# Kernel tuning notes

Measured on AMD Instinct MI355X. Metric: run time of the kernel, lower is better.

The kernel has to match this reference:

```python
import jax, jax.numpy as jnp
import numpy as np

Y_DIM = 100  # number of speakers (one-hot dim)


def _conv1d(x, w, b, stride=2, pad=1):
    # x: [B, Cin, L], w: [Cout, Cin, K] (torch Conv1d layout)
    out = jax.lax.conv_general_dilated(x, w, (stride,), [(pad, pad)],
                                       dimension_numbers=('NCH', 'OIH', 'NCH'))
    return out + b[None, :, None]


def _deconv1d(x, w, b, stride=2, pad=1):
    # w: [Cin, Cout, K] (torch ConvTranspose1d layout)
    k = w.shape[-1]
    wt = jnp.flip(w, -1).transpose(1, 0, 2)  # -> [Cout, Cin, K]
    out = jax.lax.conv_general_dilated(x, wt, (1,), [(k - 1 - pad, k - 1 - pad)],
                                       lhs_dilation=(stride,),
                                       dimension_numbers=('NCH', 'OIH', 'NCH'))
    return out + b[None, :, None]


def _forward(x, enc, codebook, emb_w, emb_b, dec, mu_w, mu_b, spk_idx):
    h = x[:, None, :]                         # [B, 1, 512]
    for w, b in enc:
        h = jax.nn.relu(_conv1d(h, w, b))
    z = h[:, 0, :]                            # [B, 64]
    # 0.5 * ||z - c||^2 for all codes, via expansion (fused cdist)
    d = 0.5 * (jnp.sum(z * z, 1, keepdims=True)
               - 2.0 * z @ codebook.T
               + jnp.sum(codebook * codebook, 1)[None, :])  # [B, K]
    idx = jnp.argmin(d, axis=1)               # first-min tie-break matches strict '<' loop
    code = codebook[idx]                      # [B, 64]
    y = jax.nn.one_hot(spk_idx, Y_DIM, dtype=x.dtype)
    dec_in = jnp.concatenate([code, y], 1) @ emb_w.T + emb_b  # [B, 64]
    h = dec_in[:, None, :]
    for w, b in dec:
        h = jax.nn.relu(_deconv1d(h, w, b))
    out = (h @ mu_w.T + mu_b)[:, 0, :]        # [B, 512]
    return z, code, out


def setup_inputs() -> dict:
    key = jax.random.key(0)
    ks = jax.random.split(key, 20)
    B, L, D, K, Y = 8192, 512, 64, 512, 100
    s = 0.1
    return {
        'x': jax.random.normal(ks[0], (B, L), jnp.float32),
        'enc_w0': jax.random.normal(ks[1], (32, 1, 4), jnp.float32) * s,
        'enc_b0': jnp.zeros((32,), jnp.float32),
        'enc_w1': jax.random.normal(ks[2], (32, 32, 4), jnp.float32) * s,
        'enc_b1': jnp.zeros((32,), jnp.float32),
        'enc_w2': jax.random.normal(ks[3], (1, 32, 4), jnp.float32) * s,
        'enc_b2': jnp.zeros((1,), jnp.float32),
        'codebook': jax.random.normal(ks[4], (K, D), jnp.float32) * s,
        'emb_w': jax.random.normal(ks[5], (D, Y + D), jnp.float32) * s,
        'emb_b': jnp.zeros((D,), jnp.float32),
        'dec_w0': jax.random.normal(ks[6], (1, 32, 4), jnp.float32) * s,
        'dec_b0': jnp.zeros((32,), jnp.float32),
        'dec_w1': jax.random.normal(ks[7], (32, 32, 4), jnp.float32) * s,
        'dec_b1': jnp.zeros((32,), jnp.float32),
        'dec_w2': jax.random.normal(ks[8], (32, 1, 4), jnp.float32) * s,
        'dec_b2': jnp.zeros((1,), jnp.float32),
        'mu_w': jax.random.normal(ks[9], (L, L), jnp.float32) * s,
        'mu_b': jnp.zeros((L,), jnp.float32),
        'spk_idx': jax.random.randint(ks[10], (B,), 0, Y, jnp.int32),
    }


def reference(x, enc_w0, enc_b0, enc_w1, enc_b1, enc_w2, enc_b2, codebook,
              emb_w, emb_b, dec_w0, dec_b0, dec_w1, dec_b1, dec_w2, dec_b2,
              mu_w, mu_b, spk_idx):
    enc = [(enc_w0, enc_b0), (enc_w1, enc_b1), (enc_w2, enc_b2)]
    dec = [(dec_w0, dec_b0), (dec_w1, dec_b1), (dec_w2, dec_b2)]
    return _forward(x, enc, codebook, emb_w, emb_b, dec, mu_w, mu_b, spk_idx)
```

## Files before the change

kernel.cpp:

```cpp
#include <hip/hip_runtime.h>
#include <hip/hip_bf16.h>

__device__ __forceinline__ float bits2f(unsigned int b) {
    union { unsigned int u; float f; } v; v.u = b; return v.f;
}
__device__ __forceinline__ unsigned short f2bf_bits(float f) {
    union { float f; unsigned int u; } v; v.f = f;
    return (unsigned short)((v.u + 0x7fffu + ((v.u >> 16) & 1u)) >> 16);
}
__device__ __forceinline__ unsigned short f2h_bits(_Float16 h) {
    union { _Float16 f; unsigned short u; } v; v.f = h; return v.u;
}

typedef __attribute__((ext_vector_type(8))) short short8;
typedef __attribute__((ext_vector_type(4))) float f32x4;
typedef _Float16 f16x8 __attribute__((ext_vector_type(8)));

#define AS1 __attribute__((address_space(1)))
#define AS3 __attribute__((address_space(3)))

__device__ __align__(16) unsigned short g_muwb[512 * 512];
__device__ __align__(16) unsigned short g_dec1B[4096];
__device__ __align__(16) unsigned short g_dec2B[5120];
__device__ __align__(16) unsigned short g_encBh[4096];
__device__ __align__(16) unsigned short g_encBl[4096];
__device__ float g_cc[512];
__device__ __align__(16) float g_cbT[64 * 512];
__device__ __align__(16) float g_embwT[164 * 64];

__global__ __launch_bounds__(256)
void k_prep(const float* __restrict__ muw, const float* __restrict__ dw1,
            const float* __restrict__ dw2, const float* __restrict__ ew1,
            const float* __restrict__ cb, const float* __restrict__ embw)
{
    int idx = blockIdx.x * 256 + threadIdx.x;
    if (idx < 262144) { g_muwb[idx] = f2bf_bits(muw[idx]); return; }
    int e = idx - 262144;
    if (e < 4096) {
        const int jsel[4] = {1, 3, 2, 0};
        int pt = e >> 10, o = (e >> 5) & 31, i = e & 31;
        g_dec1B[e] = f2bf_bits(dw1[i * 128 + o * 4 + jsel[pt]]);
        return;
    }
    int f = e - 4096;
    if (f < 5120) {
        int j = f / 320, k = f - j * 320;
        int lam = k >> 5, i = k & 31, q = j >> 1;
        float v = 0.f;
        if ((j & 1) == 0) {
            if (lam == q + 1) v = dw2[4 * i + 1];
            else if (lam == q) v = dw2[4 * i + 3];
        } else {
            if (lam == q + 1) v = dw2[4 * i + 2];
            else if (lam == q + 2) v = dw2[4 * i + 0];
        }
        g_dec2B[f] = f2bf_bits(v);
        return;
    }
    int g = f - 5120;
    if (g < 4096) {
        int j = g >> 10, o = (g >> 5) & 31, i = g & 31;
        float w = ew1[o * 128 + i * 4 + j];
        _Float16 wh = (_Float16)w;
        _Float16 wl = (_Float16)((w - (float)wh) * 2048.0f);
        g_encBh[g] = f2h_bits(wh);
        g_encBl[g] = f2h_bits(wl);
        return;
    }
    int h = g - 4096;
    if (h < 512) {
        const float4* cp = (const float4*)(cb + (size_t)h * 64);
        float cc2 = 0.f;
        #pragma unroll
        for (int q = 0; q < 16; ++q) {
            float4 u = cp[q];
            cc2 += u.x * u.x + u.y * u.y + u.z * u.z + u.w * u.w;
        }
        g_cc[h] = cc2;
        return;
    }
    int m = h - 512;
    if (m < 32768) {
        int d = m >> 9, c = m & 511;
        g_cbT[m] = cb[(size_t)c * 64 + d];
        return;
    }
    int n2 = m - 32768;
    if (n2 < 10496) {
        int k = n2 >> 6, j = n2 & 63;
        g_embwT[n2] = embw[(size_t)j * 164 + k];
    }
}

__global__ __launch_bounds__(256, 2)
void k_encoder(const float* __restrict__ x,
               const float* __restrict__ ew0, const float* __restrict__ eb0,
               const float* __restrict__ eb1,
               const float* __restrict__ ew2, const float* __restrict__ eb2,
               float* __restrict__ z_out)
{
    const int tid  = threadIdx.x;
    const int lane = tid & 63;
    const int w    = tid >> 6;
    const int rloc = w >> 1;
    const int wh   = w & 1;
    const int row  = blockIdx.x * 2 + rloc;

    __shared__ __align__(16) float POOL[2 * 4688];
    float* ws = POOL + rloc * 4688;
    float* xs = ws;
    float* h2 = ws + 520;

    const int r = lane & 15, kc = lane >> 4;
    const float biaN0 = eb1[r], biaN1 = eb1[16 + r];

    const float* xrow = x + (size_t)row * 512;
    #pragma unroll
    for (int q = 0; q < 4; ++q) {
        const int ch = wh * 4 + q;
        xs[3 + lane + 64 * ch] = xrow[lane + 64 * ch];
    }
    if (wh == 0) {
        if (lane < 3) xs[lane] = 0.f;
        h2[(lane >> 1) * 130 + 2 + (lane & 1)] = 0.f;
    } else {
        if (lane < 3) xs[515 + lane] = 0.f;
        if (lane < 2) { int gi = 64 + lane; h2[(gi >> 1) * 130 + 2 + (gi & 1)] = 0.f; }
    }

    f16x8 Bh[2][4], Bl[2][4];
    #pragma unroll
    for (int nt = 0; nt < 2; ++nt)
        #pragma unroll
        for (int j = 0; j < 4; ++j) {
            const int off = (j * 32 + nt * 16 + r) * 32 + kc * 8;
            Bh[nt][j] = *(const f16x8*)(g_encBh + off);
            Bl[nt][j] = *(const f16x8*)(g_encBl + off);
        }
    float4 Wv[8]; float b0v[8];
    #pragma unroll
    for (int i = 0; i < 8; ++i) {
        Wv[i]  = *(const float4*)(ew0 + (kc * 8 + i) * 4);
        b0v[i] = eb0[kc * 8 + i];
    }
    __syncthreads();

    #pragma unroll 2
    for (int mi = 0; mi < 4; ++mi) {
        const int m = 4 * wh + mi;
        const int t2 = m * 16 + r;
        float xw[10];
        {
            const float* xwin = xs + 4 * t2;
            #pragma unroll
            for (int q = 0; q < 10; ++q) xw[q] = xwin[q];
        }
        f16x8 ah0, ah1, ah2, ah3, al0, al1, al2, al3;
        #pragma unroll
        for (int i = 0; i < 8; ++i) {
            const float4 W = Wv[i];
            const float b0 = b0v[i];
            float v0 = fmaxf(b0 + xw[0] * W.x + xw[1] * W.y + xw[2] * W.z + xw[3] * W.w, 0.f);
            float v1 = fmaxf(b0 + xw[2] * W.x + xw[3] * W.y + xw[4] * W.z + xw[5] * W.w, 0.f);
            float v2 = fmaxf(b0 + xw[4] * W.x + xw[5] * W.y + xw[6] * W.z + xw[7] * W.w, 0.f);
            float v3 = fmaxf(b0 + xw[6] * W.x + xw[7] * W.y + xw[8] * W.z + xw[9] * W.w, 0.f);
            _Float16 hh0 = (_Float16)v0, hh1 = (_Float16)v1;
            _Float16 hh2 = (_Float16)v2, hh3 = (_Float16)v3;
            _Float16 ll0 = (_Float16)((v0 - (float)hh0) * 2048.0f);
            _Float16 ll1 = (_Float16)((v1 - (float)hh1) * 2048.0f);
            _Float16 ll2 = (_Float16)((v2 - (float)hh2) * 2048.0f);
            _Float16 ll3 = (_Float16)((v3 - (float)hh3) * 2048.0f);
            ah0[i] = hh0; al0[i] = ll0;
            ah1[i] = hh1; al1[i] = ll1;
            ah2[i] = hh2; al2[i] = ll2;
            ah3[i] = hh3; al3[i] = ll3;
        }
        {
            const f16x8 Z8 = {(_Float16)0.f, (_Float16)0.f, (_Float16)0.f, (_Float16)0.f,
                              (_Float16)0.f, (_Float16)0.f, (_Float16)0.f, (_Float16)0.f};
            if (t2 == 0)   { ah0 = Z8; al0 = Z8; }
            if (t2 == 127) { ah3 = Z8; al3 = Z8; }
        }
        const int t0 = m * 16;
        #pragma unroll
        for (int nt = 0; nt < 2; ++nt) {
            f32x4 ahh = (f32x4){0.f, 0.f, 0.f, 0.f};
            f32x4 am  = (f32x4){0.f, 0.f, 0.f, 0.f};
            f32x4 all_= (f32x4){0.f, 0.f, 0.f, 0.f};
            ahh = __builtin_amdgcn_mfma_f32_16x16x32_f16(ah0, Bh[nt][0], ahh, 0, 0, 0);
            am  = __builtin_amdgcn_mfma_f32_16x16x32_f16(ah0, Bl[nt][0], am,  0, 0, 0);
            am  = __builtin_amdgcn_mfma_f32_16x16x32_f16(al0, Bh[nt][0], am,  0, 0, 0);
            all_= __builtin_amdgcn_mfma_f32_16x16x32_f16(al0, Bl[nt][0], all_,0, 0, 0);
            ahh = __builtin_amdgcn_mfma_f32_16x16x32_f16(ah1, Bh[nt][1], ahh, 0, 0, 0);
            am  = __builtin_amdgcn_mfma_f32_16x16x32_f16(ah1, Bl[nt][1], am,  0, 0, 0);
            am  = __builtin_amdgcn_mfma_f32_16x16x32_f16(al1, Bh[nt][1], am,  0, 0, 0);
            all_= __builtin_amdgcn_mfma_f32_16x16x32_f16(al1, Bl[nt][1], all_,0, 0, 0);
            ahh = __builtin_amdgcn_mfma_f32_16x16x32_f16(ah2, Bh[nt][2], ahh, 0, 0, 0);
            am  = __builtin_amdgcn_mfma_f32_16x16x32_f16(ah2, Bl[nt][2], am,  0, 0, 0);
            am  = __builtin_amdgcn_mfma_f32_16x16x32_f16(al2, Bh[nt][2], am,  0, 0, 0);
            all_= __builtin_amdgcn_mfma_f32_16x16x32_f16(al2, Bl[nt][2], all_,0, 0, 0);
            ahh = __builtin_amdgcn_mfma_f32_16x16x32_f16(ah3, Bh[nt][3], ahh, 0, 0, 0);
            am  = __builtin_amdgcn_mfma_f32_16x16x32_f16(ah3, Bl[nt][3], am,  0, 0, 0);
            am  = __builtin_amdgcn_mfma_f32_16x16x32_f16(al3, Bh[nt][3], am,  0, 0, 0);
            all_= __builtin_amdgcn_mfma_f32_16x16x32_f16(al3, Bl[nt][3], all_,0, 0, 0);
            const float bia = nt ? biaN1 : biaN0;
            float* orow = h2 + (nt * 16 + r) * 130 + 4 + t0 + kc * 4;
            #pragma unroll
            for (int e = 0; e < 4; ++e)
                orow[e] = fmaxf(ahh[e] + 4.8828125e-4f * am[e]
                                + 2.384185791015625e-07f * all_[e] + bia, 0.f);
        }
    }
    __syncthreads();

    if (wh == 0) {
        const int t = lane;
        float pg[4];
        #pragma unroll
        for (int gg = 0; gg < 4; ++gg) {
            float p = 0.f;
            #pragma unroll
            for (int ii = 0; ii < 8; ++ii) {
                const int i = gg * 8 + ii;
                const float4 W = *(const float4*)(ew2 + i * 4);
                const float* hr = h2 + i * 130 + 4;
                p += hr[2 * t - 1] * W.x + hr[2 * t] * W.y
                   + hr[2 * t + 1] * W.z + hr[2 * t + 2] * W.w;
            }
            pg[gg] = p;
        }
        float zv = fmaxf(pg[0] + pg[1] + pg[2] + pg[3] + eb2[0], 0.f);
        z_out[(size_t)row * 64 + t] = zv;
    }
}

__global__ __launch_bounds__(256)
void k_enc_tail(const float* __restrict__ z_in, const float* __restrict__ cb,
                const float* __restrict__ embb,
                const int* __restrict__ spk,
                float* __restrict__ code_out, float* __restrict__ din_g)
{
    const int blk  = blockIdx.x;
    const int tid  = threadIdx.x;
    const int lane = tid & 63;
    const int wv   = tid >> 6;

    __shared__ __align__(16) float zs[8][64];
    __shared__ __align__(16) float csf[8][64];
    __shared__ float zzv[8];
    __shared__ float redv[4][8];
    __shared__ int   redi[4][8];
    __shared__ int   sidxs[8];

    const int jq = tid & 63;
    const int rq = tid >> 6;

    #pragma unroll
    for (int ch = 0; ch < 2; ++ch) {
        const int rr = rq + ch * 4;
        zs[rr][jq] = z_in[((size_t)blk * 8 + rr) * 64 + jq];
    }
    __syncthreads();

    if (tid < 8) {
        float4 zr[16];
        #pragma unroll
        for (int q = 0; q < 16; ++q) zr[q] = *(const float4*)(&zs[tid][4 * q]);
        float u[32];
        #pragma unroll
        for (int q = 0; q < 8; ++q) {
            u[4 * q + 0] = __fadd_rn(__fmul_rn(zr[q].x, zr[q].x), __fmul_rn(zr[q + 8].x, zr[q + 8].x));
            u[4 * q + 1] = __fadd_rn(__fmul_rn(zr[q].y, zr[q].y), __fmul_rn(zr[q + 8].y, zr[q + 8].y));
            u[4 * q + 2] = __fadd_rn(__fmul_rn(zr[q].z, zr[q].z), __fmul_rn(zr[q + 8].z, zr[q + 8].z));
            u[4 * q + 3] = __fadd_rn(__fmul_rn(zr[q].w, zr[q].w), __fmul_rn(zr[q + 8].w, zr[q + 8].w));
        }
        #pragma unroll
        for (int off = 16; off; off >>= 1)
            #pragma unroll
            for (int i = 0; i < off; ++i) u[i] = __fadd_rn(u[i], u[i + off]);
        zzv[tid] = u[0];
    }

    float acc[8][2];
    #pragma unroll
    for (int r2 = 0; r2 < 8; ++r2) { acc[r2][0] = 0.f; acc[r2][1] = 0.f; }

    #pragma unroll 4
    for (int dq = 0; dq < 16; ++dq) {
        float4 zv[8];
        #pragma unroll
        for (int r2 = 0; r2 < 8; ++r2) zv[r2] = *(const float4*)(&zs[r2][4 * dq]);
        #pragma unroll
        for (int dd = 0; dd < 4; ++dd) {
            const int d = 4 * dq + dd;
            const float w0 = g_cbT[d * 512 + tid];
            const float w1 = g_cbT[d * 512 + 256 + tid];
            #pragma unroll
            for (int r2 = 0; r2 < 8; ++r2) {
                const float zd = (dd == 0) ? zv[r2].x : (dd == 1) ? zv[r2].y
                               : (dd == 2) ? zv[r2].z : zv[r2].w;
                acc[r2][0] = fmaf(w0, zd, acc[r2][0]);
                acc[r2][1] = fmaf(w1, zd, acc[r2][1]);
            }
        }
    }
    __syncthreads();

    {
        const float cc0 = g_cc[tid], cc1 = g_cc[tid + 256];
        float best[8]; int bidx[8];
        #pragma unroll
        for (int r2 = 0; r2 < 8; ++r2) {
            const float zz = zzv[r2];
            float d0 = 0.5f * (zz - 2.f * acc[r2][0] + cc0);
            float d1 = 0.5f * (zz - 2.f * acc[r2][1] + cc1);
            best[r2] = d0; bidx[r2] = tid;
            if (d1 < best[r2]) { best[r2] = d1; bidx[r2] = tid + 256; }
        }
        #pragma unroll
        for (int off = 32; off; off >>= 1) {
            #pragma unroll
            for (int r2 = 0; r2 < 8; ++r2) {
                float od = __shfl_down(best[r2], off);
                int   oi = __shfl_down(bidx[r2], off);
                if (od < best[r2] || (od == best[r2] && oi < bidx[r2])) {
                    best[r2] = od; bidx[r2] = oi;
                }
            }
        }
        if (lane == 0) {
            #pragma unroll
            for (int r2 = 0; r2 < 8; ++r2) { redv[wv][r2] = best[r2]; redi[wv][r2] = bidx[r2]; }
        }
    }
    __syncthreads();
    if (tid < 8) {
        float bd = redv[0][tid]; int bi = redi[0][tid];
        #pragma unroll
        for (int w = 1; w < 4; ++w)
            if (redv[w][tid] < bd || (redv[w][tid] == bd && redi[w][tid] < bi)) {
                bd = redv[w][tid]; bi = redi[w][tid];
            }
        sidxs[tid] = min(max(bi, 0), 511);
    }
    __syncthreads();

    #pragma unroll
    for (int ch = 0; ch < 2; ++ch) {
        const int rr = rq + ch * 4;
        const int sx = sidxs[rr];
        const float cv = cb[(size_t)sx * 64 + jq];
        code_out[((size_t)blk * 8 + rr) * 64 + jq] = cv;
        csf[rr][jq] = cv;
    }
    __syncthreads();
    #pragma unroll
    for (int ch = 0; ch < 2; ++ch) {
        const int rr = rq + ch * 4;
        const size_t b2 = (size_t)blk * 8 + rr;
        float pg[4];
        #pragma unroll
        for (int gg = 0; gg < 4; ++gg) {
            float p = 0.f;
            #pragma unroll
            for (int q = 0; q < 4; ++q) {
                const int k0 = 16 * gg + 4 * q;
                const float w0 = g_embwT[(k0 + 0) * 64 + jq];
                const float w1 = g_embwT[(k0 + 1) * 64 + jq];
                const float w2 = g_embwT[(k0 + 2) * 64 + jq];
                const float w3 = g_embwT[(k0 + 3) * 64 + jq];
                p += w0 * csf[rr][k0 + 0] + w1 * csf[rr][k0 + 1]
                   + w2 * csf[rr][k0 + 2] + w3 * csf[rr][k0 + 3];
            }
            pg[gg] = p;
        }
        float a = pg[0] + pg[1] + pg[2] + pg[3]
                + embb[jq] + g_embwT[(64 + spk[b2]) * 64 + jq];
        din_g[b2 * 64 + jq] = a;
    }
}

__global__ __launch_bounds__(256)
void k_decoder(const float* __restrict__ din_g,
               const float* __restrict__ dw0, const float* __restrict__ db0,
               const float* __restrict__ db1, const float* __restrict__ db2,
               unsigned short* __restrict__ hdec)
{
    const int gidx = blockIdx.x;
    const int bblk = gidx >> 4;
    const int m0   = ((gidx >> 1) & 7) * 16;
    const int hh   = gidx & 1;
    const int tid  = threadIdx.x;
    const int lane = tid & 63;
    const int wid  = tid >> 6;

    __shared__ __align__(16) float        dins[16 * 68];
    __shared__ __align__(16) unsigned int d1c[10 * 16 * 18];
    __shared__ __align__(16) unsigned int d2c[18 * 16 * 18];

    {
        int b = tid >> 4, j4 = tid & 15;
        float4 v = *(const float4*)(din_g + ((size_t)bblk * 16 + b) * 64 + j4 * 4);
        float* dr = dins + b * 68 + 1 + j4 * 4;
        dr[0] = v.x; dr[1] = v.y; dr[2] = v.z; dr[3] = v.w;
        if (j4 == 0) { dins[b * 68] = 0.f; dins[b * 68 + 65] = 0.f; }
    }
    const int i2h = tid & 15;
    const float4 Wa = *(const float4*)(dw0 + 8 * i2h);
    const float4 Wb = *(const float4*)(dw0 + 8 * i2h + 4);
    const float ba0 = db0[2 * i2h], ba1 = db0[2 * i2h + 1];
    const float bia2 = db2[0];

    const int r = lane & 15, kc = lane >> 4;
    const int pw = (wid & 1) ^ 1;
    const unsigned short* Bp = g_dec1B + pw * 2048;
    const short8 B00 = *(const short8*)(Bp + (r) * 32 + kc * 8);
    const short8 B10 = *(const short8*)(Bp + 1024 + (r) * 32 + kc * 8);
    const short8 B01 = *(const short8*)(Bp + (16 + r) * 32 + kc * 8);
    const short8 B11 = *(const short8*)(Bp + 1024 + (16 + r) * 32 + kc * 8);
    const float bv0 = db1[r], bv1 = db1[16 + r];
    __syncthreads();

    #pragma unroll 5
    for (int it = 0; it < 10; ++it) {
        int b = (tid >> 4) & 15;
        int tau = 8 * hh + it;
        int s = m0 - 1 + tau;
        unsigned int pk = 0u;
        if (s >= 0 && s < 128) {
            const float* dn = dins + b * 68 + 1;
            int m = s >> 1;
            float v0, v1;
            if (s & 1) { v0 = ba0 + dn[m] * Wa.z + dn[m + 1] * Wa.x;
                         v1 = ba1 + dn[m] * Wb.z + dn[m + 1] * Wb.x; }
            else       { v0 = ba0 + dn[m] * Wa.y + dn[m - 1] * Wa.w;
                         v1 = ba1 + dn[m] * Wb.y + dn[m - 1] * Wb.w; }
            pk = (unsigned int)f2bf_bits(fmaxf(v0, 0.f))
               | ((unsigned int)f2bf_bits(fmaxf(v1, 0.f)) << 16);
        }
        d1c[it * 288 + b * 18 + i2h] = pk;
    }
    __syncthreads();

    {
        const unsigned short* d1u = (const unsigned short*)d1c;
        unsigned short* d2u = (unsigned short*)d2c;
        for (int sgl = wid; sgl < 18; sgl += 4) {
            int t = 2 * m0 - 1 + 16 * hh + sgl;
            f32x4 acc0 = (f32x4){0.f, 0.f, 0.f, 0.f};
            f32x4 acc1 = (f32x4){0.f, 0.f, 0.f, 0.f};
            if (t >= 0 && t < 256) {
                int tauAl = (sgl + 1) >> 1;
                int tauBl = pw ? tauAl + 1 : tauAl - 1;
                short8 Am = *(const short8*)(d1u + tauAl * 576 + r * 36 + kc * 8);
                short8 Ap = *(const short8*)(d1u + tauBl * 576 + r * 36 + kc * 8);
                acc0 = __builtin_amdgcn_mfma_f32_16x16x32_bf16(Am, B00, acc0, 0, 0, 0);
                acc0 = __builtin_amdgcn_mfma_f32_16x16x32_bf16(Ap, B10, acc0, 0, 0, 0);
                acc1 = __builtin_amdgcn_mfma_f32_16x16x32_bf16(Am, B01, acc1, 0, 0, 0);
                acc1 = __builtin_amdgcn_mfma_f32_16x16x32_bf16(Ap, B11, acc1, 0, 0, 0);
                #pragma unroll
                for (int e = 0; e < 4; ++e) {
                    int bC = kc * 4 + e;
                    d2u[sgl * 576 + bC * 36 + r]      = f2bf_bits(fmaxf(acc0[e] + bv0, 0.f));
                    d2u[sgl * 576 + bC * 36 + 16 + r] = f2bf_bits(fmaxf(acc1[e] + bv1, 0.f));
                }
            } else {
                #pragma unroll
                for (int e = 0; e < 4; ++e) {
                    int bC = kc * 4 + e;
                    d2u[sgl * 576 + bC * 36 + r]      = 0;
                    d2u[sgl * 576 + bC * 36 + 16 + r] = 0;
                }
            }
        }
    }
    __syncthreads();

    if (wid < 2) {
        const unsigned short* d2u = (const unsigned short*)d2c;
        const int sig0 = 8 * wid;
        f32x4 acc = (f32x4){0.f, 0.f, 0.f, 0.f};
        #pragma unroll
        for (int kap = 0; kap < 10; ++kap) {
            short8 A = *(const short8*)(d2u + (sig0 + kap) * 576 + r * 36 + kc * 8);
            short8 B = *(const short8*)(g_dec2B + r * 320 + kap * 32 + kc * 8);
            acc = __builtin_amdgcn_mfma_f32_16x16x32_bf16(A, B, acc, 0, 0, 0);
        }
        const int n = 4 * m0 + 32 * hh + 16 * wid + r;
        #pragma unroll
        for (int e = 0; e < 4; ++e) {
            int b = kc * 4 + e;
            hdec[((size_t)bblk * 16 + b) * 512 + n] = f2bf_bits(fmaxf(acc[e] + bia2, 0.f));
        }
    }
}

__global__ __launch_bounds__(256)
void k_mu_gemm(const unsigned short* __restrict__ A,
               const float* __restrict__ bias,
               float* __restrict__ C)
{
    __shared__ unsigned short As[128 * 32];
    __shared__ unsigned short Bs[128 * 32];
    const int tid  = threadIdx.x;
    const int lane = tid & 63;
    const int wid  = tid >> 6;
    const int bm   = blockIdx.x & 63;
    const int bn   = blockIdx.x >> 6;
    const int wm   = (wid & 1) * 64;
    const int wn   = (wid >> 1) * 64;
    const unsigned short* Ab = A + (size_t)bm * 128 * 512;
    const unsigned short* Bb = g_muwb + (size_t)bn * 128 * 512;

    f32x4 acc[4][4];
    #pragma unroll
    for (int i = 0; i < 4; ++i)
        #pragma unroll
        for (int j = 0; j < 4; ++j)
            acc[i][j] = (f32x4){0.f, 0.f, 0.f, 0.f};

    const int r  = lane & 15;
    const int kc = lane >> 4;

    for (int ks = 0; ks < 16; ++ks) {
        const int k0 = ks * 32;
        #pragma unroll
        for (int q = 0; q < 2; ++q) {
            const int off  = q * 4096 + tid * 16;
            const int row  = off >> 6;
            const int colb = off & 63;
            const char* ga = (const char*)Ab + (size_t)row * 1024 + (size_t)k0 * 2 + colb;
            const char* gb = (const char*)Bb + (size_t)row * 1024 + (size_t)k0 * 2 + colb;
            char* la = (char*)As + q * 4096 + wid * 1024;
            char* lb = (char*)Bs + q * 4096 + wid * 1024;
            __builtin_amdgcn_global_load_lds((AS1 const unsigned int*)ga, (AS3 unsigned int*)la, 16, 0, 0);
            __builtin_amdgcn_global_load_lds((AS1 const unsigned int*)gb, (AS3 unsigned int*)lb, 16, 0, 0);
        }
        __syncthreads();

        short8 af[4], bf[4];
        #pragma unroll
        for (int mf = 0; mf < 4; ++mf)
            af[mf] = *(const short8*)&As[(wm + mf * 16 + r) * 32 + kc * 8];
        #pragma unroll
        for (int nf = 0; nf < 4; ++nf)
            bf[nf] = *(const short8*)&Bs[(wn + nf * 16 + r) * 32 + kc * 8];
        #pragma unroll
        for (int mf = 0; mf < 4; ++mf)
            #pragma unroll
            for (int nf = 0; nf < 4; ++nf)
                acc[mf][nf] = __builtin_amdgcn_mfma_f32_16x16x32_bf16(af[mf], bf[nf], acc[mf][nf], 0, 0, 0);
        __syncthreads();
    }

    const int col = lane & 15;
    const int rg  = lane >> 4;
    float bv[4];
    #pragma unroll
    for (int nf = 0; nf < 4; ++nf)
        bv[nf] = bias[bn * 128 + wn + nf * 16 + col];
    #pragma unroll
    for (int mf = 0; mf < 4; ++mf)
        #pragma unroll
        for (int nf = 0; nf < 4; ++nf)
            #pragma unroll
            for (int e = 0; e < 4; ++e) {
                int m = bm * 128 + wm + mf * 16 + rg * 4 + e;
                int n = bn * 128 + wn + nf * 16 + col;
                C[(size_t)m * 512 + n] = acc[mf][nf][e] + bv[nf];
            }
}

extern "C" void kernel_launch(void* const* d_in, const int* in_sizes, int n_in,
                              void* d_out, int out_size, void* d_ws, size_t ws_size,
                              hipStream_t stream) {
    const float* x    = (const float*)d_in[0];
    const float* ew0  = (const float*)d_in[1];
    const float* eb0  = (const float*)d_in[2];
    const float* ew1  = (const float*)d_in[3];
    const float* eb1  = (const float*)d_in[4];
    const float* ew2  = (const float*)d_in[5];
    const float* eb2  = (const float*)d_in[6];
    const float* cb   = (const float*)d_in[7];
    const float* embw = (const float*)d_in[8];
    const float* embb = (const float*)d_in[9];
    const float* dw0  = (const float*)d_in[10];
    const float* db0  = (const float*)d_in[11];
    const float* dw1  = (const float*)d_in[12];
    const float* db1  = (const float*)d_in[13];
    const float* dw2  = (const float*)d_in[14];
    const float* db2  = (const float*)d_in[15];
    const float* muw  = (const float*)d_in[16];
    const float* mub  = (const float*)d_in[17];
    const int*   spk  = (const int*)d_in[18];

    float* zout = (float*)d_out;
    float* cout = zout + (size_t)8192 * 64;
    float* yout = zout + (size_t)2 * 8192 * 64;
    float* din_g = zout + (size_t)8192 * 576;

    unsigned short* hdec = (unsigned short*)d_ws;

    k_prep<<<dim3(1247), dim3(256), 0, stream>>>(muw, dw1, dw2, ew1, cb, embw);

    k_encoder<<<dim3(4096), dim3(256), 0, stream>>>(
        x, ew0, eb0, eb1, ew2, eb2, zout);

    k_enc_tail<<<dim3(1024), dim3(256), 0, stream>>>(
        zout, cb, embb, spk, cout, din_g);

    k_decoder<<<dim3(8192), dim3(256), 0, stream>>>(din_g, dw0, db0, db1, db2, hdec);

    k_mu_gemm<<<dim3(256), dim3(256), 0, stream>>>(hdec, mub, yout);
}
```

Baseline: 179.0 us.

## Restructure decoder so each wave computes its own slice without block barriers

Each block of the decoder kernel now covers a full 16-position m-tile instead of half, so the grid is halved. Each wave computes its own layer-1 deconv outputs directly into registers, laid out as MFMA A operands. It then runs layer 2 into a private shared-memory slice and layer 3 from that slice, which removes the shared d1 buffer and two block-wide barriers. In exchange there is redundant layer-1 compute across waves (6 positions per 4 outputs), more registers for weights and B fragments, and more LDS per block.

New measurement: 159.3 us. -11.0%, faster.

```diff
diff --git a/kernel.cpp b/kernel.cpp
--- a/kernel.cpp
+++ b/kernel.cpp
@@ -387,16 +387,14 @@
                unsigned short* __restrict__ hdec)
 {
     const int gidx = blockIdx.x;
-    const int bblk = gidx >> 4;
-    const int m0   = ((gidx >> 1) & 7) * 16;
-    const int hh   = gidx & 1;
+    const int bblk = gidx >> 3;
+    const int m0   = (gidx & 7) * 16;
     const int tid  = threadIdx.x;
     const int lane = tid & 63;
-    const int wid  = tid >> 6;
+    const int q    = tid >> 6;
 
     __shared__ __align__(16) float        dins[16 * 68];
-    __shared__ __align__(16) unsigned int d1c[10 * 16 * 18];
-    __shared__ __align__(16) unsigned int d2c[18 * 16 * 18];
+    __shared__ __align__(16) unsigned int d2c[4][10 * 16 * 18];
 
     {
         int b = tid >> 4, j4 = tid & 15;
@@ -405,88 +403,99 @@
         dr[0] = v.x; dr[1] = v.y; dr[2] = v.z; dr[3] = v.w;
         if (j4 == 0) { dins[b * 68] = 0.f; dins[b * 68 + 65] = 0.f; }
     }
-    const int i2h = tid & 15;
-    const float4 Wa = *(const float4*)(dw0 + 8 * i2h);
-    const float4 Wb = *(const float4*)(dw0 + 8 * i2h + 4);
-    const float ba0 = db0[2 * i2h], ba1 = db0[2 * i2h + 1];
+
+    const int r = lane & 15, kc = lane >> 4;
     const float bia2 = db2[0];
 
-    const int r = lane & 15, kc = lane >> 4;
-    const int pw = (wid & 1) ^ 1;
-    const unsigned short* Bp = g_dec1B + pw * 2048;
-    const short8 B00 = *(const short8*)(Bp + (r) * 32 + kc * 8);
-    const short8 B10 = *(const short8*)(Bp + 1024 + (r) * 32 + kc * 8);
-    const short8 B01 = *(const short8*)(Bp + (16 + r) * 32 + kc * 8);
-    const short8 B11 = *(const short8*)(Bp + 1024 + (16 + r) * 32 + kc * 8);
+    float4 Wa[4], Wb[4]; float ba0v[4], ba1v[4];
+    #pragma unroll
+    for (int j = 0; j < 4; ++j) {
+        const int pp = 4 * kc + j;
+        Wa[j] = *(const float4*)(dw0 + 8 * pp);
+        Wb[j] = *(const float4*)(dw0 + 8 * pp + 4);
+        ba0v[j] = db0[2 * pp];
+        ba1v[j] = db0[2 * pp + 1];
+    }
+    short8 B00[2], B10[2], B01[2], B11[2];
+    #pragma unroll
+    for (int p = 0; p < 2; ++p) {
+        const unsigned short* Bp = g_dec1B + p * 2048;
+        B00[p] = *(const short8*)(Bp + (r) * 32 + kc * 8);
+        B10[p] = *(const short8*)(Bp + 1024 + (r) * 32 + kc * 8);
+        B01[p] = *(const short8*)(Bp + (16 + r) * 32 + kc * 8);
+        B11[p] = *(const short8*)(Bp + 1024 + (16 + r) * 32 + kc * 8);
+    }
     const float bv0 = db1[r], bv1 = db1[16 + r];
     __syncthreads();
 
-    #pragma unroll 5
-    for (int it = 0; it < 10; ++it) {
-        int b = (tid >> 4) & 15;
-        int tau = 8 * hh + it;
-        int s = m0 - 1 + tau;
-        unsigned int pk = 0u;
-        if (s >= 0 && s < 128) {
-            const float* dn = dins + b * 68 + 1;
-            int m = s >> 1;
-            float v0, v1;
-            if (s & 1) { v0 = ba0 + dn[m] * Wa.z + dn[m + 1] * Wa.x;
-                         v1 = ba1 + dn[m] * Wb.z + dn[m + 1] * Wb.x; }
-            else       { v0 = ba0 + dn[m] * Wa.y + dn[m - 1] * Wa.w;
-                         v1 = ba1 + dn[m] * Wb.y + dn[m - 1] * Wb.w; }
-            pk = (unsigned int)f2bf_bits(fmaxf(v0, 0.f))
-               | ((unsigned int)f2bf_bits(fmaxf(v1, 0.f)) << 16);
-        }
-        d1c[it * 288 + b * 18 + i2h] = pk;
-    }
-    __syncthreads();
-
-    {
-        const unsigned short* d1u = (const unsigned short*)d1c;
-        unsigned short* d2u = (unsigned short*)d2c;
-        for (int sgl = wid; sgl < 18; sgl += 4) {
-            int t = 2 * m0 - 1 + 16 * hh + sgl;
+    unsigned int d1r[6][4];
+    const float* dn = dins + r * 68 + 1;
+    #pragma unroll
+    for (int tl = 0; tl < 6; ++tl) {
+        const int s = m0 - 1 + 4 * q + tl;
+        const bool inb = (s >= 0 && s < 128);
+        const int m = s >> 1;
+        #pragma unroll
+        for (int j = 0; j < 4; ++j) {
+            unsigned int pk = 0u;
+            if (inb) {
+                float v0, v1;
+                if (s & 1) { v0 = ba0v[j] + dn[m] * Wa[j].z + dn[m + 1] * Wa[j].x;
+                             v1 = ba1v[j] + dn[m] * Wb[j].z + dn[m + 1] * Wb[j].x; }
+                else       { v0 = ba0v[j] + dn[m] * Wa[j].y + dn[m - 1] * Wa[j].w;
+                             v1 = ba1v[j] + dn[m] * Wb[j].y + dn[m - 1] * Wb[j].w; }
+                pk = (unsigned int)f2bf_bits(fmaxf(v0, 0.f))
+                   | ((unsigned int)f2bf_bits(fmaxf(v1, 0.f)) << 16);
+            }
+            d1r[tl][j] = pk;
+        }
+    }
+
+    unsigned short* d2u = (unsigned short*)(d2c[q]);
+    const int tb = 2 * m0 - 1 + 8 * q;
+    #pragma unroll
+    for (int sgl = 0; sgl < 10; ++sgl) {
+        const int p     = 1 - (sgl & 1);
+        const int tauAl = (sgl + 1) >> 1;
+        const int tauBl = p ? tauAl + 1 : tauAl - 1;
+        const int t = tb + sgl;
+        if (t >= 0 && t < 256) {
+            union { unsigned int u[4]; short8 s8; } am_, ap_;
+            am_.u[0] = d1r[tauAl][0]; am_.u[1] = d1r[tauAl][1];
+            am_.u[2] = d1r[tauAl][2]; am_.u[3] = d1r[tauAl][3];
+            ap_.u[0] = d1r[tauBl][0]; ap_.u[1] = d1r[tauBl][1];
+            ap_.u[2] = d1r[tauBl][2]; ap_.u[3] = d1r[tauBl][3];
             f32x4 acc0 = (f32x4){0.f, 0.f, 0.f, 0.f};
             f32x4 acc1 = (f32x4){0.f, 0.f, 0.f, 0.f};
-            if (t >= 0 && t < 256) {
-                int tauAl = (sgl + 1) >> 1;
-                int tauBl = pw ? tauAl + 1 : tauAl - 1;
-                short8 Am = *(const short8*)(d1u + tauAl * 576 + r * 36 + kc * 8);
-                short8 Ap = *(const short8*)(d1u + tauBl * 576 + r * 36 + kc * 8);
-                acc0 = __builtin_amdgcn_mfma_f32_16x16x32_bf16(Am, B00, acc0, 0, 0, 0);
-                acc0 = __builtin_amdgcn_mfma_f32_16x16x32_bf16(Ap, B10, acc0, 0, 0, 0);
-                acc1 = __builtin_amdgcn_mfma_f32_16x16x32_bf16(Am, B01, acc1, 0, 0, 0);
-                acc1 = __builtin_amdgcn_mfma_f32_16x16x32_bf16(Ap, B11, acc1, 0, 0, 0);
-                #pragma unroll
-                for (int e = 0; e < 4; ++e) {
-                    int bC = kc * 4 + e;
-                    d2u[sgl * 576 + bC * 36 + r]      = f2bf_bits(fmaxf(acc0[e] + bv0, 0.f));
-                    d2u[sgl * 576 + bC * 36 + 16 + r] = f2bf_bits(fmaxf(acc1[e] + bv1, 0.f));
-                }
-            } else {
-                #pragma unroll
-                for (int e = 0; e < 4; ++e) {
-                    int bC = kc * 4 + e;
-                    d2u[sgl * 576 + bC * 36 + r]      = 0;
-                    d2u[sgl * 576 + bC * 36 + 16 + r] = 0;
-                }
-            }
-        }
-    }
-    __syncthreads();
-
-    if (wid < 2) {
-        const unsigned short* d2u = (const unsigned short*)d2c;
-        const int sig0 = 8 * wid;
+            acc0 = __builtin_amdgcn_mfma_f32_16x16x32_bf16(am_.s8, B00[p], acc0, 0, 0, 0);
+            acc0 = __builtin_amdgcn_mfma_f32_16x16x32_bf16(ap_.s8, B10[p], acc0, 0, 0, 0);
+            acc1 = __builtin_amdgcn_mfma_f32_16x16x32_bf16(am_.s8, B01[p], acc1, 0, 0, 0);
+            acc1 = __builtin_amdgcn_mfma_f32_16x16x32_bf16(ap_.s8, B11[p], acc1, 0, 0, 0);
+            #pragma unroll
+            for (int e = 0; e < 4; ++e) {
+                int bC = kc * 4 + e;
+                d2u[sgl * 576 + bC * 36 + r]      = f2bf_bits(fmaxf(acc0[e] + bv0, 0.f));
+                d2u[sgl * 576 + bC * 36 + 16 + r] = f2bf_bits(fmaxf(acc1[e] + bv1, 0.f));
+            }
+        } else {
+            #pragma unroll
+            for (int e = 0; e < 4; ++e) {
+                int bC = kc * 4 + e;
+                d2u[sgl * 576 + bC * 36 + r]      = 0;
+                d2u[sgl * 576 + bC * 36 + 16 + r] = 0;
+            }
+        }
+    }
+
+    {
         f32x4 acc = (f32x4){0.f, 0.f, 0.f, 0.f};
         #pragma unroll
         for (int kap = 0; kap < 10; ++kap) {
-            short8 A = *(const short8*)(d2u + (sig0 + kap) * 576 + r * 36 + kc * 8);
+            short8 A = *(const short8*)(d2u + kap * 576 + r * 36 + kc * 8);
             short8 B = *(const short8*)(g_dec2B + r * 320 + kap * 32 + kc * 8);
             acc = __builtin_amdgcn_mfma_f32_16x16x32_bf16(A, B, acc, 0, 0, 0);
         }
-        const int n = 4 * m0 + 32 * hh + 16 * wid + r;
+        const int n = 4 * m0 + 16 * q + r;
         #pragma unroll
         for (int e = 0; e < 4; ++e) {
             int b = kc * 4 + e;
@@ -609,7 +618,7 @@
     k_enc_tail<<<dim3(1024), dim3(256), 0, stream>>>(
         zout, cb, embb, spk, cout, din_g);
 
-    k_decoder<<<dim3(8192), dim3(256), 0, stream>>>(din_g, dw0, db0, db1, db2, hdec);
+    k_decoder<<<dim3(4096), dim3(256), 0, stream>>>(din_g, dw0, db0, db1, db2, hdec);
 
     k_mu_gemm<<<dim3(256), dim3(256), 0, stream>>>(hdec, mub, yout);
 }
```
